# Kernel tuning notes

Measured on AMD Instinct MI355X. Metric: run time of the kernel, lower is better.

Reference implementation:

```python
import jax, jax.numpy as jnp
import numpy as np

NUM_HEADS = 16
HEAD_DIM = 64
Q_DIM = K_DIM = V_DIM = 1024
LQ = LK = 4096
TAU = HEAD_DIM ** (-0.5)


def setup_inputs() -> dict:
    key = jax.random.key(0)
    ks = jax.random.split(key, 11)
    inner = NUM_HEADS * HEAD_DIM
    s = 0.02
    return {
        "q": jax.random.normal(ks[0], (LQ, Q_DIM), dtype=jnp.float32),
        "k": jax.random.normal(ks[1], (LK, K_DIM), dtype=jnp.float32),
        "v": jax.random.normal(ks[2], (LK, V_DIM), dtype=jnp.float32),
        "Wq": jax.random.normal(ks[3], (Q_DIM, inner), dtype=jnp.float32) * s,
        "bq": jax.random.normal(ks[4], (inner,), dtype=jnp.float32) * s,
        "Wk": jax.random.normal(ks[5], (K_DIM, inner), dtype=jnp.float32) * s,
        "bk": jax.random.normal(ks[6], (inner,), dtype=jnp.float32) * s,
        "Wv": jax.random.normal(ks[7], (V_DIM, inner), dtype=jnp.float32) * s,
        "bv": jax.random.normal(ks[8], (inner,), dtype=jnp.float32) * s,
        "Wo": jax.random.normal(ks[9], (inner, Q_DIM), dtype=jnp.float32) * s,
        "bo": jax.random.normal(ks[10], (Q_DIM,), dtype=jnp.float32) * s,
    }


def reference(q, k, v, Wq, bq, Wk, bk, Wv, bv, Wo, bo):
    h, x = NUM_HEADS, HEAD_DIM
    # projections: [L, h*x] -> per-head layout
    qh = (q @ Wq + bq).reshape(-1, h, x)  # [Lq, h, x]
    kh = (k @ Wk + bk).reshape(-1, h, x)  # [Lk, h, x]
    vh = (v @ Wv + bv).reshape(-1, h, x)  # [Lk, h, x]
    # scores: [h, Lq, Lk]
    att = jnp.einsum('qhx,khx->hqk', qh, kh) * TAU
    att = jax.nn.softmax(att, axis=-1)  # dropout=0.0 -> identity
    ctx = jnp.einsum('hqk,khx->qhx', att, vh).reshape(-1, h * x)  # [Lq, h*x]
    out = ctx @ Wo + bo  # [Lq, Q_DIM]
    return out, att
```

## Files before the change

kernel.cpp:

```cpp
#include <hip/hip_runtime.h>
#include <hip/hip_bf16.h>

typedef unsigned short ushort_t;
typedef __attribute__((ext_vector_type(8))) short short8;
typedef __attribute__((ext_vector_type(8))) __bf16 bf16x8;
typedef __attribute__((ext_vector_type(4))) float f32x4;

#define LQS 4096
#define LKS 4096
#define NH 16
#define HD 64
#define DIN 1024
#define QBLK 64
#define KVB 64
static constexpr float TAU_S = 0.125f;
static constexpr float LOG2E = 1.4426950408889634f;

__device__ __forceinline__ float exp2_fast(float x) { return __builtin_amdgcn_exp2f(x); }
__device__ __forceinline__ float log2_fast(float x) { return __builtin_amdgcn_logf(x); }

__device__ __forceinline__ ushort_t f32_to_bf16(float x) {
  union { float f; unsigned u; } v; v.f = x;
  unsigned r = v.u + 0x7FFF + ((v.u >> 16) & 1);
  return (ushort_t)(r >> 16);
}

__device__ __forceinline__ unsigned cvt_pk_bf16(float a, float b) {
  unsigned r;
  asm volatile("v_cvt_pk_bf16_f32 %0, %1, %2" : "=v"(r) : "v"(a), "v"(b));
  return r;
}

__device__ __forceinline__ void gld_lds16(const void* g, void* l) {
  __builtin_amdgcn_global_load_lds((const __attribute__((address_space(1))) void*)g,
                                   (__attribute__((address_space(3))) void*)l, 16, 0, 0);
}

__device__ __forceinline__ f32x4 mfma16(bf16x8 a, bf16x8 b, f32x4 c) {
  return __builtin_amdgcn_mfma_f32_16x16x32_bf16(a, b, c, 0, 0, 0);
}

struct Cvt3 { const float* src[3]; ushort_t* dst[3]; };
__global__ void cvt_kernel(Cvt3 c) {
  const float* __restrict__ src = c.src[blockIdx.y];
  ushort_t* __restrict__ dst = c.dst[blockIdx.y];
  int i = (blockIdx.x * 256 + threadIdx.x) * 8;
  float4 a = *(const float4*)(src + i);
  float4 b = *(const float4*)(src + i + 4);
  union { unsigned w[4]; short8 s; } o;
  o.w[0] = cvt_pk_bf16(a.x, a.y);
  o.w[1] = cvt_pk_bf16(a.z, a.w);
  o.w[2] = cvt_pk_bf16(b.x, b.y);
  o.w[3] = cvt_pk_bf16(b.z, b.w);
  *(short8*)(dst + i) = o.s;
}

struct TW4 { const float* W[4]; ushort_t* Wt[4]; };
__global__ void transpose_w(TW4 w) {
  const float* __restrict__ W = w.W[blockIdx.z];
  ushort_t* __restrict__ Wt = w.Wt[blockIdx.z];
  __shared__ float tile[64][65];
  const int t = threadIdx.x;
  const int k0 = blockIdx.y * 64, n0 = blockIdx.x * 64;
#pragma unroll
  for (int i = 0; i < 16; ++i) {
    int idx = i * 256 + t;
    int r = idx >> 6, c = idx & 63;
    tile[r][c] = W[(size_t)(k0 + r) * DIN + n0 + c];
  }
  __syncthreads();
#pragma unroll
  for (int i = 0; i < 16; ++i) {
    int idx = i * 256 + t;
    int r = idx >> 6, c = idx & 63;
    Wt[(size_t)(n0 + r) * DIN + k0 + c] = f32_to_bf16(tile[c][r]);
  }
}

__global__ void transpose_v(const ushort_t* __restrict__ vh, ushort_t* __restrict__ vt) {
  __shared__ ushort_t tile[64][65];
  const int t = threadIdx.x;
  const int k0 = blockIdx.x * 64, h = blockIdx.y;
#pragma unroll
  for (int i = 0; i < 16; ++i) {
    int idx = i * 256 + t;
    int r = idx >> 6, c = idx & 63;
    tile[r][c] = vh[(size_t)(k0 + r) * DIN + h * HD + c];
  }
  __syncthreads();
#pragma unroll
  for (int i = 0; i < 16; ++i) {
    int idx = i * 256 + t;
    int r = idx >> 6, c = idx & 63;
    vt[((size_t)h * HD + r) * (size_t)LKS + k0 + c] = tile[c][r];
  }
}

struct Batch3 {
  const ushort_t* A[3];
  const ushort_t* Bt[3];
  const float* bias[3];
  void* C[3];
  float scale[3];
};
template <bool OUT_F32>
__launch_bounds__(256, 2)
__global__ void gemm_nt(Batch3 bt3) {
  const int bid = blockIdx.x;
  const int xcd = bid & 7, idx = bid >> 3;
  const int z = idx >> 5, rem = idx & 31;
  const int by = xcd * 4 + (rem >> 3), bx = rem & 7;
  const ushort_t* __restrict__ A = bt3.A[z];
  const ushort_t* __restrict__ Bt = bt3.Bt[z];
  const float* __restrict__ bias = bt3.bias[z];
  void* __restrict__ Cout = bt3.C[z];
  const float scale = bt3.scale[z];
  const int K = DIN, N = DIN;

  __shared__ __align__(16) ushort_t Alds[128 * 64];
  __shared__ __align__(16) ushort_t Blds[128 * 64];
  const int t = threadIdx.x, wave = t >> 6, lane = t & 63;
  const int l15 = lane & 15, lg = lane >> 4;
  const int m0 = by * 128, n0 = bx * 128;
  const int wr = wave >> 1, wc = wave & 1;
  f32x4 acc[4][4];
#pragma unroll
  for (int i = 0; i < 4; ++i)
#pragma unroll
    for (int j = 0; j < 4; ++j) acc[i][j] = (f32x4){0.f, 0.f, 0.f, 0.f};

  for (int tk = 0; tk < K / 64; ++tk) {
#pragma unroll
    for (int c = 0; c < 4; ++c) {
      int chunk = wave * 4 + c;
      int row = chunk * 8 + (lane >> 3);
      int ss = (lane & 7) ^ (row & 7);
      gld_lds16(A + (size_t)(m0 + row) * K + tk * 64 + ss * 8, (char*)Alds + chunk * 1024);
      gld_lds16(Bt + (size_t)(n0 + row) * K + tk * 64 + ss * 8, (char*)Blds + chunk * 1024);
    }
    __syncthreads();
#pragma unroll
    for (int kk = 0; kk < 2; ++kk) {
      bf16x8 a[4], b[4];
#pragma unroll
      for (int i = 0; i < 4; ++i) {
        int ra = wr * 64 + i * 16 + l15;
        a[i] = *(const bf16x8*)((const char*)Alds + ra * 128 + ((((kk * 4 + lg) << 4)) ^ ((ra & 7) << 4)));
        int rb = wc * 64 + i * 16 + l15;
        b[i] = *(const bf16x8*)((const char*)Blds + rb * 128 + ((((kk * 4 + lg) << 4)) ^ ((rb & 7) << 4)));
      }
#pragma unroll
      for (int mi = 0; mi < 4; ++mi)
#pragma unroll
        for (int ni = 0; ni < 4; ++ni)
          acc[mi][ni] = mfma16(a[mi], b[ni], acc[mi][ni]);
    }
    __syncthreads();
  }
#pragma unroll
  for (int ni = 0; ni < 4; ++ni) {
    int coln = n0 + wc * 64 + ni * 16 + l15;
    float bv = bias[coln];
#pragma unroll
    for (int mi = 0; mi < 4; ++mi) {
#pragma unroll
      for (int r = 0; r < 4; ++r) {
        int rowm = m0 + wr * 64 + mi * 16 + lg * 4 + r;
        float v = (acc[mi][ni][r] + bv) * scale;
        if (OUT_F32)
          ((float*)Cout)[(size_t)rowm * N + coln] = v;
        else
          ((ushort_t*)Cout)[(size_t)rowm * N + coln] = f32_to_bf16(v);
      }
    }
  }
}

__launch_bounds__(256, 4)
__global__ void attn_kernel(const ushort_t* __restrict__ qh, const ushort_t* __restrict__ kh,
                            const ushort_t* __restrict__ vt, float* __restrict__ att,
                            ushort_t* __restrict__ ctx) {
  __shared__ __align__(16) ushort_t Klds[2][KVB * 64];
  __shared__ __align__(16) ushort_t Vlds[2][KVB * 64];
  const int t = threadIdx.x, wave = t >> 6, lane = t & 63;
  const int l15 = lane & 15, lg = lane >> 4;
  const int bid = blockIdx.x;
  const int xcd = bid & 7, idx = bid >> 3;
  const int h = xcd * 2 + (idx >> 6);
  const int q0 = (idx & 63) * QBLK;
  const int w0 = q0 + wave * 16;

  bf16x8 qa[2];
  {
    const ushort_t* qp = qh + (size_t)(w0 + l15) * DIN + h * HD + lg * 8;
    qa[0] = *(const bf16x8*)(qp);
    qa[1] = *(const bf16x8*)(qp + 32);
  }

  const int srow8 = lane >> 3;
  const int sslot = (lane & 7);

  float rs_lane = 0.f;
  for (int tk = 0; tk < LKS / (2 * KVB); ++tk) {
#pragma unroll
    for (int sub = 0; sub < 2; ++sub) {
#pragma unroll
      for (int c = 0; c < 2; ++c) {
        int chunk = wave * 2 + c;
        int row = chunk * 8 + srow8;
        int ss = sslot ^ (row & 7);
        gld_lds16(kh + (size_t)((tk * 2 + sub) * KVB + row) * DIN + h * HD + ss * 8,
                  (char*)Klds[sub] + chunk * 1024);
      }
    }
    __syncthreads();
#pragma unroll
    for (int sub = 0; sub < 2; ++sub) {
#pragma unroll
      for (int ct = 0; ct < 4; ++ct) {
        f32x4 acc = (f32x4){0.f, 0.f, 0.f, 0.f};
#pragma unroll
        for (int kk = 0; kk < 2; ++kk) {
          int row = ct * 16 + l15;
          bf16x8 kb = *(const bf16x8*)((const char*)Klds[sub] + row * 128 + ((((kk * 4 + lg) << 4)) ^ ((row & 7) << 4)));
          acc = mfma16(kb, qa[kk], acc);
        }
#pragma unroll
        for (int r = 0; r < 4; ++r) rs_lane += exp2_fast(acc[r]);
      }
    }
    __syncthreads();
  }
  rs_lane += __shfl_xor(rs_lane, 16, 64);
  rs_lane += __shfl_xor(rs_lane, 32, 64);
  const float lrs = log2_fast(rs_lane);

  f32x4 cacc[4];
#pragma unroll
  for (int x = 0; x < 4; ++x) cacc[x] = (f32x4){0.f, 0.f, 0.f, 0.f};
  float* atth = att + ((size_t)h << 24);

  for (int tk = 0; tk < LKS / (2 * KVB); ++tk) {
#pragma unroll
    for (int sub = 0; sub < 2; ++sub) {
#pragma unroll
      for (int c = 0; c < 2; ++c) {
        int chunk = wave * 2 + c;
        int row = chunk * 8 + srow8;
        int ss = sslot ^ (row & 7);
        gld_lds16(kh + (size_t)((tk * 2 + sub) * KVB + row) * DIN + h * HD + ss * 8,
                  (char*)Klds[sub] + chunk * 1024);
        gld_lds16(vt + ((size_t)h * HD + row) * (size_t)LKS + (tk * 2 + sub) * KVB + ss * 8,
                  (char*)Vlds[sub] + chunk * 1024);
      }
    }
    __syncthreads();
#pragma unroll
    for (int sub = 0; sub < 2; ++sub) {
      float p[4][4];
#pragma unroll
      for (int ct = 0; ct < 4; ++ct) {
        f32x4 acc = (f32x4){0.f, 0.f, 0.f, 0.f};
#pragma unroll
        for (int kk = 0; kk < 2; ++kk) {
          int row = ct * 16 + l15;
          bf16x8 kb = *(const bf16x8*)((const char*)Klds[sub] + row * 128 + ((((kk * 4 + lg) << 4)) ^ ((row & 7) << 4)));
          acc = mfma16(kb, qa[kk], acc);
        }
#pragma unroll
        for (int r = 0; r < 4; ++r) p[ct][r] = exp2_fast(acc[r] - lrs);
      }
#pragma unroll
      for (int ct = 0; ct < 4; ++ct) {
        f32x4 v = (f32x4){p[ct][0], p[ct][1], p[ct][2], p[ct][3]};
        *(f32x4*)(atth + (((size_t)(w0 + l15)) << 12) + (tk * 2 + sub) * KVB + ct * 16 + lg * 4) = v;
      }
      bf16x8 pa[2];
#pragma unroll
      for (int kk = 0; kk < 2; ++kk) {
        union { unsigned w[4]; bf16x8 v; } P;
        P.w[0] = cvt_pk_bf16(p[2 * kk][0], p[2 * kk][1]);
        P.w[1] = cvt_pk_bf16(p[2 * kk][2], p[2 * kk][3]);
        P.w[2] = cvt_pk_bf16(p[2 * kk + 1][0], p[2 * kk + 1][1]);
        P.w[3] = cvt_pk_bf16(p[2 * kk + 1][2], p[2 * kk + 1][3]);
        pa[kk] = P.v;
      }
#pragma unroll
      for (int x = 0; x < 4; ++x) {
        int row = x * 16 + l15;
        const char* vrow = (const char*)Vlds[sub] + row * 128;
        int par = row & 7;
        int sb = (lg & 1) << 3;
#pragma unroll
        for (int kk = 0; kk < 2; ++kk) {
          int sA = (4 * kk + (lg >> 1)) ^ par;
          int sB = (4 * kk + 2 + (lg >> 1)) ^ par;
          union { unsigned long long q[2]; bf16x8 v; } U;
          U.q[0] = *(const unsigned long long*)(vrow + (sA << 4) + sb);
          U.q[1] = *(const unsigned long long*)(vrow + (sB << 4) + sb);
          cacc[x] = mfma16(pa[kk], U.v, cacc[x]);
        }
      }
    }
    __syncthreads();
  }
#pragma unroll
  for (int x = 0; x < 4; ++x) {
#pragma unroll
    for (int r = 0; r < 4; ++r) {
      int rowq = w0 + lg * 4 + r;
      int col = h * HD + x * 16 + l15;
      ctx[(size_t)rowq * DIN + col] = f32_to_bf16(cacc[x][r]);
    }
  }
}

extern "C" void kernel_launch(void* const* d_in, const int* in_sizes, int n_in,
                              void* d_out, int out_size, void* d_ws, size_t ws_size,
                              hipStream_t stream) {
  const float* q = (const float*)d_in[0];
  const float* k = (const float*)d_in[1];
  const float* v = (const float*)d_in[2];
  const float* Wq = (const float*)d_in[3];
  const float* bq = (const float*)d_in[4];
  const float* Wk = (const float*)d_in[5];
  const float* bk = (const float*)d_in[6];
  const float* Wv = (const float*)d_in[7];
  const float* bv = (const float*)d_in[8];
  const float* Wo = (const float*)d_in[9];
  const float* bo = (const float*)d_in[10];

  float* out = (float*)d_out;
  float* att = out + (size_t)LQS * DIN;

  char* ws = (char*)d_ws;
  ushort_t* qhb = (ushort_t*)(ws + (size_t)0);
  ushort_t* khb = (ushort_t*)(ws + ((size_t)8 << 20));
  ushort_t* vhb = (ushort_t*)(ws + ((size_t)16 << 20));
  ushort_t* vtb = (ushort_t*)(ws + ((size_t)24 << 20));
  ushort_t* ctx = (ushort_t*)(ws + ((size_t)32 << 20));
  ushort_t* qb = (ushort_t*)(ws + ((size_t)40 << 20));
  ushort_t* kb = (ushort_t*)(ws + ((size_t)48 << 20));
  ushort_t* vb = (ushort_t*)(ws + ((size_t)56 << 20));
  ushort_t* Wqt = (ushort_t*)(ws + ((size_t)64 << 20));
  ushort_t* Wkt = (ushort_t*)(ws + ((size_t)66 << 20));
  ushort_t* Wvt = (ushort_t*)(ws + ((size_t)68 << 20));
  ushort_t* Wot = (ushort_t*)(ws + ((size_t)70 << 20));

  Cvt3 c3;
  c3.src[0] = q; c3.src[1] = k; c3.src[2] = v;
  c3.dst[0] = qb; c3.dst[1] = kb; c3.dst[2] = vb;
  cvt_kernel<<<dim3(LQS * DIN / 8 / 256, 3), 256, 0, stream>>>(c3);

  TW4 w4;
  w4.W[0] = Wq; w4.W[1] = Wk; w4.W[2] = Wv; w4.W[3] = Wo;
  w4.Wt[0] = Wqt; w4.Wt[1] = Wkt; w4.Wt[2] = Wvt; w4.Wt[3] = Wot;
  transpose_w<<<dim3(16, 16, 4), 256, 0, stream>>>(w4);

  Batch3 pb;
  pb.A[0] = qb; pb.A[1] = kb; pb.A[2] = vb;
  pb.Bt[0] = Wqt; pb.Bt[1] = Wkt; pb.Bt[2] = Wvt;
  pb.bias[0] = bq; pb.bias[1] = bk; pb.bias[2] = bv;
  pb.C[0] = qhb; pb.C[1] = khb; pb.C[2] = vhb;
  pb.scale[0] = TAU_S * LOG2E; pb.scale[1] = 1.0f; pb.scale[2] = 1.0f;
  gemm_nt<false><<<768, 256, 0, stream>>>(pb);

  transpose_v<<<dim3(64, 16), 256, 0, stream>>>(vhb, vtb);

  attn_kernel<<<1024, 256, 0, stream>>>(qhb, khb, vtb, att, ctx);

  Batch3 ob;
  ob.A[0] = ctx; ob.A[1] = ctx; ob.A[2] = ctx;
  ob.Bt[0] = Wot; ob.Bt[1] = Wot; ob.Bt[2] = Wot;
  ob.bias[0] = bo; ob.bias[1] = bo; ob.bias[2] = bo;
  ob.C[0] = out; ob.C[1] = out; ob.C[2] = out;
  ob.scale[0] = 1.0f; ob.scale[1] = 1.0f; ob.scale[2] = 1.0f;
  gemm_nt<true><<<256, 256, 0, stream>>>(ob);
}
```

Measured before the change: 427.0 us.

## Process two 16-row query groups per wave in attention kernel

Each wave now handles 32 query rows instead of 16, so each block covers 128 queries and the grid is halved to 512 blocks. Every K and V fragment read from LDS now feeds two MFMAs, and each K/V tile loaded from global memory serves twice as many queries. This roughly halves K/V global traffic and LDS reads per query. In exchange it raises register pressure, so launch bounds drop to 2 blocks per CU, and there are fewer blocks to cover latency.

```diff
diff --git a/kernel.cpp b/kernel.cpp
--- a/kernel.cpp
+++ b/kernel.cpp
@@ -11,7 +11,6 @@
 #define NH 16
 #define HD 64
 #define DIN 1024
-#define QBLK 64
 #define KVB 64
 static constexpr float TAU_S = 0.125f;
 static constexpr float LOG2E = 1.4426950408889634f;
@@ -176,7 +175,7 @@
   }
 }
 
-__launch_bounds__(256, 4)
+__launch_bounds__(256, 2)
 __global__ void attn_kernel(const ushort_t* __restrict__ qh, const ushort_t* __restrict__ kh,
                             const ushort_t* __restrict__ vt, float* __restrict__ att,
                             ushort_t* __restrict__ ctx) {
@@ -186,21 +185,22 @@
   const int l15 = lane & 15, lg = lane >> 4;
   const int bid = blockIdx.x;
   const int xcd = bid & 7, idx = bid >> 3;
-  const int h = xcd * 2 + (idx >> 6);
-  const int q0 = (idx & 63) * QBLK;
-  const int w0 = q0 + wave * 16;
-
-  bf16x8 qa[2];
-  {
-    const ushort_t* qp = qh + (size_t)(w0 + l15) * DIN + h * HD + lg * 8;
-    qa[0] = *(const bf16x8*)(qp);
-    qa[1] = *(const bf16x8*)(qp + 32);
+  const int h = xcd * 2 + (idx >> 5);
+  const int q0 = (idx & 31) * 128;
+  const int w0 = q0 + wave * 32;
+
+  bf16x8 qa[2][2];
+#pragma unroll
+  for (int g = 0; g < 2; ++g) {
+    const ushort_t* qp = qh + (size_t)(w0 + g * 16 + l15) * DIN + h * HD + lg * 8;
+    qa[g][0] = *(const bf16x8*)(qp);
+    qa[g][1] = *(const bf16x8*)(qp + 32);
   }
 
   const int srow8 = lane >> 3;
   const int sslot = (lane & 7);
 
-  float rs_lane = 0.f;
+  float rs[2] = {0.f, 0.f};
   for (int tk = 0; tk < LKS / (2 * KVB); ++tk) {
 #pragma unroll
     for (int sub = 0; sub < 2; ++sub) {
@@ -218,26 +218,37 @@
     for (int sub = 0; sub < 2; ++sub) {
 #pragma unroll
       for (int ct = 0; ct < 4; ++ct) {
-        f32x4 acc = (f32x4){0.f, 0.f, 0.f, 0.f};
+        f32x4 a0 = (f32x4){0.f, 0.f, 0.f, 0.f};
+        f32x4 a1 = (f32x4){0.f, 0.f, 0.f, 0.f};
 #pragma unroll
         for (int kk = 0; kk < 2; ++kk) {
           int row = ct * 16 + l15;
           bf16x8 kb = *(const bf16x8*)((const char*)Klds[sub] + row * 128 + ((((kk * 4 + lg) << 4)) ^ ((row & 7) << 4)));
-          acc = mfma16(kb, qa[kk], acc);
-        }
-#pragma unroll
-        for (int r = 0; r < 4; ++r) rs_lane += exp2_fast(acc[r]);
-      }
-    }
-    __syncthreads();
-  }
-  rs_lane += __shfl_xor(rs_lane, 16, 64);
-  rs_lane += __shfl_xor(rs_lane, 32, 64);
-  const float lrs = log2_fast(rs_lane);
-
-  f32x4 cacc[4];
-#pragma unroll
-  for (int x = 0; x < 4; ++x) cacc[x] = (f32x4){0.f, 0.f, 0.f, 0.f};
+          a0 = mfma16(kb, qa[0][kk], a0);
+          a1 = mfma16(kb, qa[1][kk], a1);
+        }
+#pragma unroll
+        for (int r = 0; r < 4; ++r) {
+          rs[0] += exp2_fast(a0[r]);
+          rs[1] += exp2_fast(a1[r]);
+        }
+      }
+    }
+    __syncthreads();
+  }
+  float lrs[2];
+#pragma unroll
+  for (int g = 0; g < 2; ++g) {
+    rs[g] += __shfl_xor(rs[g], 16, 64);
+    rs[g] += __shfl_xor(rs[g], 32, 64);
+    lrs[g] = log2_fast(rs[g]);
+  }
+
+  f32x4 cacc[2][4];
+#pragma unroll
+  for (int g = 0; g < 2; ++g)
+#pragma unroll
+    for (int x = 0; x < 4; ++x) cacc[g][x] = (f32x4){0.f, 0.f, 0.f, 0.f};
   float* atth = att + ((size_t)h << 24);
 
   for (int tk = 0; tk < LKS / (2 * KVB); ++tk) {
@@ -257,34 +268,44 @@
     __syncthreads();
 #pragma unroll
     for (int sub = 0; sub < 2; ++sub) {
-      float p[4][4];
+      float p[2][4][4];
 #pragma unroll
       for (int ct = 0; ct < 4; ++ct) {
-        f32x4 acc = (f32x4){0.f, 0.f, 0.f, 0.f};
+        f32x4 a0 = (f32x4){0.f, 0.f, 0.f, 0.f};
+        f32x4 a1 = (f32x4){0.f, 0.f, 0.f, 0.f};
 #pragma unroll
         for (int kk = 0; kk < 2; ++kk) {
           int row = ct * 16 + l15;
           bf16x8 kb = *(const bf16x8*)((const char*)Klds[sub] + row * 128 + ((((kk * 4 + lg) << 4)) ^ ((row & 7) << 4)));
-          acc = mfma16(kb, qa[kk], acc);
-        }
-#pragma unroll
-        for (int r = 0; r < 4; ++r) p[ct][r] = exp2_fast(acc[r] - lrs);
-      }
-#pragma unroll
-      for (int ct = 0; ct < 4; ++ct) {
-        f32x4 v = (f32x4){p[ct][0], p[ct][1], p[ct][2], p[ct][3]};
-        *(f32x4*)(atth + (((size_t)(w0 + l15)) << 12) + (tk * 2 + sub) * KVB + ct * 16 + lg * 4) = v;
-      }
-      bf16x8 pa[2];
-#pragma unroll
-      for (int kk = 0; kk < 2; ++kk) {
-        union { unsigned w[4]; bf16x8 v; } P;
-        P.w[0] = cvt_pk_bf16(p[2 * kk][0], p[2 * kk][1]);
-        P.w[1] = cvt_pk_bf16(p[2 * kk][2], p[2 * kk][3]);
-        P.w[2] = cvt_pk_bf16(p[2 * kk + 1][0], p[2 * kk + 1][1]);
-        P.w[3] = cvt_pk_bf16(p[2 * kk + 1][2], p[2 * kk + 1][3]);
-        pa[kk] = P.v;
-      }
+          a0 = mfma16(kb, qa[0][kk], a0);
+          a1 = mfma16(kb, qa[1][kk], a1);
+        }
+#pragma unroll
+        for (int r = 0; r < 4; ++r) {
+          p[0][ct][r] = exp2_fast(a0[r] - lrs[0]);
+          p[1][ct][r] = exp2_fast(a1[r] - lrs[1]);
+        }
+      }
+#pragma unroll
+      for (int g = 0; g < 2; ++g) {
+#pragma unroll
+        for (int ct = 0; ct < 4; ++ct) {
+          f32x4 v = (f32x4){p[g][ct][0], p[g][ct][1], p[g][ct][2], p[g][ct][3]};
+          *(f32x4*)(atth + (((size_t)(w0 + g * 16 + l15)) << 12) + (tk * 2 + sub) * KVB + ct * 16 + lg * 4) = v;
+        }
+      }
+      bf16x8 pa[2][2];
+#pragma unroll
+      for (int g = 0; g < 2; ++g)
+#pragma unroll
+        for (int kk = 0; kk < 2; ++kk) {
+          union { unsigned w[4]; bf16x8 v; } P;
+          P.w[0] = cvt_pk_bf16(p[g][2 * kk][0], p[g][2 * kk][1]);
+          P.w[1] = cvt_pk_bf16(p[g][2 * kk][2], p[g][2 * kk][3]);
+          P.w[2] = cvt_pk_bf16(p[g][2 * kk + 1][0], p[g][2 * kk + 1][1]);
+          P.w[3] = cvt_pk_bf16(p[g][2 * kk + 1][2], p[g][2 * kk + 1][3]);
+          pa[g][kk] = P.v;
+        }
 #pragma unroll
       for (int x = 0; x < 4; ++x) {
         int row = x * 16 + l15;
@@ -298,21 +319,24 @@
           union { unsigned long long q[2]; bf16x8 v; } U;
           U.q[0] = *(const unsigned long long*)(vrow + (sA << 4) + sb);
           U.q[1] = *(const unsigned long long*)(vrow + (sB << 4) + sb);
-          cacc[x] = mfma16(pa[kk], U.v, cacc[x]);
-        }
-      }
-    }
-    __syncthreads();
-  }
-#pragma unroll
-  for (int x = 0; x < 4; ++x) {
-#pragma unroll
-    for (int r = 0; r < 4; ++r) {
-      int rowq = w0 + lg * 4 + r;
-      int col = h * HD + x * 16 + l15;
-      ctx[(size_t)rowq * DIN + col] = f32_to_bf16(cacc[x][r]);
-    }
-  }
+          cacc[0][x] = mfma16(pa[0][kk], U.v, cacc[0][x]);
+          cacc[1][x] = mfma16(pa[1][kk], U.v, cacc[1][x]);
+        }
+      }
+    }
+    __syncthreads();
+  }
+#pragma unroll
+  for (int g = 0; g < 2; ++g)
+#pragma unroll
+    for (int x = 0; x < 4; ++x) {
+#pragma unroll
+      for (int r = 0; r < 4; ++r) {
+        int rowq = w0 + g * 16 + lg * 4 + r;
+        int col = h * HD + x * 16 + l15;
+        ctx[(size_t)rowq * DIN + col] = f32_to_bf16(cacc[g][x][r]);
+      }
+    }
 }
 
 extern "C" void kernel_launch(void* const* d_in, const int* in_sizes, int n_in,
@@ -367,7 +391,7 @@
 
   transpose_v<<<dim3(64, 16), 256, 0, stream>>>(vhb, vtb);
 
-  attn_kernel<<<1024, 256, 0, stream>>>(qhb, khb, vtb, att, ctx);
+  attn_kernel<<<512, 256, 0, stream>>>(qhb, khb, vtb, att, ctx);
 
   Batch3 ob;
   ob.A[0] = ctx; ob.A[1] = ctx; ob.A[2] = ctx;
```

Result: faster. 391.6 us (-8.3%).
